# Kernel tuning notes

Hardware: AMD Instinct MI355X
Metric: run time of the kernel (lower is better)

Reference implementation:

```python
import jax, jax.numpy as jnp
import numpy as np

N = 50000       # nodes
E = 600000      # directed edges (before self loops)
IN_CH = 128
HID = 64
HEADS = 2
H2_CH = HID // HEADS  # 32
OUT_CH = 96
NEG_SLOPE = 0.2


def _w(key, shape):
    fan_in = shape[-1]
    return jax.random.normal(key, shape, dtype=jnp.float32) / np.sqrt(fan_in).astype(np.float32)


def setup_inputs() -> dict:
    key = jax.random.key(0)
    ks = jax.random.split(key, 20)
    x = jax.random.normal(ks[0], (N, IN_CH), dtype=jnp.float32)
    edge_index = jax.random.randint(ks[1], (2, E), 0, N, dtype=jnp.int32)
    batch = jnp.zeros((N,), dtype=jnp.int32)
    return {
        "x": x, "edge_index": edge_index, "batch": batch,
        # lin_in 128->128
        "Win": _w(ks[2], (IN_CH, IN_CH)), "b_in": jnp.zeros((IN_CH,), jnp.float32),
        # conv1: GATv2Conv(128 -> 64, heads=2, concat=True)
        "Wl1": _w(ks[3], (HEADS * HID, IN_CH)), "bl1": jnp.zeros((HEADS * HID,), jnp.float32),
        "Wr1": _w(ks[4], (HEADS * HID, IN_CH)), "br1": jnp.zeros((HEADS * HID,), jnp.float32),
        "att1": _w(ks[5], (HEADS, HID)), "bias1": jnp.zeros((HEADS * HID,), jnp.float32),
        # conv2: GATv2Conv(128 -> 32, heads=1, concat=True)
        "Wl2": _w(ks[6], (H2_CH, HEADS * HID)), "bl2": jnp.zeros((H2_CH,), jnp.float32),
        "Wr2": _w(ks[7], (H2_CH, HEADS * HID)), "br2": jnp.zeros((H2_CH,), jnp.float32),
        "att2": _w(ks[8], (1, H2_CH)), "bias2": jnp.zeros((H2_CH,), jnp.float32),
        # final linear 32 -> 96
        "Wout": _w(ks[9], (OUT_CH, H2_CH)), "b_out": jnp.zeros((OUT_CH,), jnp.float32),
    }


def _segment_softmax(logits, seg, num):
    # logits: [E, H] grouped by seg (destination node); every node has a self loop.
    m = jax.ops.segment_max(logits, seg, num_segments=num)
    ex = jnp.exp(logits - m[seg])
    s = jax.ops.segment_sum(ex, seg, num_segments=num)
    return ex / s[seg]


def _gatv2_conv(h, Wl, bl, Wr, br, att, bias, src, dst, heads, ch):
    n = h.shape[0]
    xl = (h @ Wl.T + bl).reshape(n, heads, ch)  # source-side (x_j)
    xr = (h @ Wr.T + br).reshape(n, heads, ch)  # target-side (x_i)
    e = jax.nn.leaky_relu(xl[src] + xr[dst], NEG_SLOPE)       # [E, H, C]
    logits = jnp.einsum('ehc,hc->eh', e, att)                  # [E, H]
    alpha = _segment_softmax(logits, dst, n)                   # softmax over in-edges per dst
    out = jax.ops.segment_sum(alpha[:, :, None] * xl[src], dst, num_segments=n)
    return out.reshape(n, heads * ch) + bias


def reference(x, edge_index, batch, Win, b_in, Wl1, bl1, Wr1, br1, att1, bias1,
              Wl2, bl2, Wr2, br2, att2, bias2, Wout, b_out):
    n = x.shape[0]
    loops = jnp.arange(n, dtype=edge_index.dtype)
    src = jnp.concatenate([edge_index[0], loops])  # add_self_loops=True (PyG default)
    dst = jnp.concatenate([edge_index[1], loops])
    h = x @ Win.T + b_in
    h = jax.nn.relu(_gatv2_conv(h, Wl1, bl1, Wr1, br1, att1, bias1, src, dst, HEADS, HID))
    h = jax.nn.relu(_gatv2_conv(h, Wl2, bl2, Wr2, br2, att2, bias2, src, dst, 1, H2_CH))
    num_graphs = 1
    sums = jax.ops.segment_sum(h, batch, num_segments=num_graphs)          # [G, 32]
    cnt = jax.ops.segment_sum(jnp.ones((n,), h.dtype), batch, num_segments=num_graphs)
    pooled = sums / cnt[:, None]
    return pooled @ Wout.T + b_out  # [G, 96]
```

## Files before the change

kernel.cpp:

```cpp
#include <hip/hip_runtime.h>
#include <hip/hip_bf16.h>
#include <math.h>


#define NEG_SLOPE 0.2f
#define LOG2E 1.4426950408889634f
#define NREP 16
#define ELLW 64
#define CH 2048
#define CAPB 8192

typedef __attribute__((ext_vector_type(8))) short bf16x8;
typedef __attribute__((ext_vector_type(4))) float f32x4;

__device__ __forceinline__ float leaky(float t) { return fmaxf(t, NEG_SLOPE * t); }
__device__ __forceinline__ float bf2f(unsigned short u) {
    return __uint_as_float((unsigned)u << 16);
}
__device__ __forceinline__ short f2bf(float f) {
    __hip_bfloat16 h = __float2bfloat16(f);
    return *reinterpret_cast<short*>(&h);
}
__device__ __forceinline__ short f2bf_fast(float f) {
    return (short)((__float_as_uint(f) + 0x8000u) >> 16);
}

__global__ __launch_bounds__(256) void prep_kernel(const float* __restrict__ Win,
                                                   const float* __restrict__ b_in,
                                                   const float* __restrict__ Wl1,
                                                   const float* __restrict__ bl1,
                                                   const float* __restrict__ Wr1,
                                                   const float* __restrict__ br1,
                                                   const float* __restrict__ Wl2,
                                                   const float* __restrict__ bl2,
                                                   const float* __restrict__ Wr2,
                                                   const float* __restrict__ br2,
                                                   unsigned short* __restrict__ Wcat1,
                                                   float* __restrict__ bcat1,
                                                   unsigned short* __restrict__ Wcat2,
                                                   float* __restrict__ bcat2,
                                                   int* __restrict__ bucketCnt,
                                                   float* __restrict__ pooledR, int N) {
    int b = blockIdx.x, t = threadIdx.x;
    if (b < 128) {
        int half = t >> 7;
        int k = t & 127;
        int o = b * 2 + half;
        const float* Wx = (o < 128) ? Wl1 : Wr1;
        const float* bx = (o < 128) ? bl1 : br1;
        int oo = o & 127;
        float acc = 0.f;
#pragma unroll 16
        for (int j = 0; j < 128; ++j)
            acc = fmaf(Wx[oo * 128 + j], Win[j * 128 + k], acc);
        Wcat1[o * 128 + k] = (unsigned short)f2bf(acc);

        __shared__ float red[256];
        red[t] = Wx[oo * 128 + k] * b_in[k];
        __syncthreads();
        for (int off = 64; off > 0; off >>= 1) {
            if (k < off) red[t] += red[t + off];
            __syncthreads();
        }
        if (k == 0) bcat1[o] = red[half * 128] + bx[oo];
    } else if (b < 160) {
        int i = (b - 128) * 256 + t;
        int m = i >> 7, kk = i & 127;
        float v = (m < 32) ? Wl2[m * 128 + kk] : Wr2[(m - 32) * 128 + kk];
        Wcat2[i] = (unsigned short)f2bf(v);
        if (b == 128 && t < 64) bcat2[t] = (t < 32) ? bl2[t] : br2[t - 32];
    } else if (b == 160) {
        if (t < 256) bucketCnt[t] = 0;
    } else {
        int i = (b - 161) * 256 + t;
        if (i < NREP * 32) pooledR[i] = 0.f;
    }
}

__global__ __launch_bounds__(256) void part_kernel(const int* __restrict__ ei,
                                                   int* __restrict__ bucketCnt,
                                                   unsigned int* __restrict__ region,
                                                   int E) {
    __shared__ int hist[256];
    __shared__ int base[256];
    __shared__ int off[256];
    int b = blockIdx.x, t = threadIdx.x;
    int e0 = b * CH;
    int e1 = e0 + CH; if (e1 > E) e1 = E;

    hist[t] = 0;
    __syncthreads();
    for (int e = e0 + t; e < e1; e += 256) {
        int d = ei[E + e];
        atomicAdd(&hist[d >> 8], 1);
    }
    __syncthreads();
    int h = hist[t];
    base[t] = (h > 0) ? atomicAdd(&bucketCnt[t], h) : 0;
    off[t] = 0;
    __syncthreads();
    for (int e = e0 + t; e < e1; e += 256) {
        int s = ei[e];
        int d = ei[E + e];
        int bk = d >> 8;
        int p = base[bk] + atomicAdd(&off[bk], 1);
        if (p < CAPB)
            region[(size_t)bk * CAPB + p] = (unsigned)s | ((unsigned)(d & 255) << 16);
    }
}

__global__ __launch_bounds__(256) void ellb_kernel(const unsigned int* __restrict__ region,
                                                   const int* __restrict__ bucketCnt,
                                                   unsigned short* __restrict__ ell,
                                                   int* __restrict__ deg, int N) {
    __shared__ unsigned short tile[256 * ELLW];
    __shared__ int cur[256];
    int nb = blockIdx.x, t = threadIdx.x;
    cur[t] = 0;
    __syncthreads();
    int cnt = bucketCnt[nb];
    if (cnt > CAPB) cnt = CAPB;
    for (int i = t; i < cnt; i += 256) {
        unsigned p = region[(size_t)nb * CAPB + i];
        int doff = p >> 16;
        int s = p & 0xFFFF;
        int r = atomicAdd(&cur[doff], 1);
        if (r < ELLW) tile[doff * ELLW + r] = (unsigned short)s;
    }
    __syncthreads();
    int node = nb * 256 + t;
    int dgl = cur[t];
    if (dgl > ELLW) dgl = ELLW;
    if (node < N) {
        deg[node] = dgl;
        int pe = dgl + 8; if (pe > ELLW) pe = ELLW;
        for (int r = dgl; r < pe; ++r) tile[t * ELLW + r] = (unsigned short)node;
    }
    __syncthreads();
    const uint4* tl = (const uint4*)tile;
    uint4* gl = (uint4*)(ell + (size_t)nb * 256 * ELLW);
#pragma unroll
    for (int k = 0; k < 8; ++k) {
        int idx = t + k * 256;
        int row = idx >> 3;
        if (nb * 256 + row < N) gl[idx] = tl[idx];
    }
}

__global__ __launch_bounds__(256) void gemm1_kernel(const float* __restrict__ x,
                                                    const unsigned short* __restrict__ W,
                                                    const float* __restrict__ bias,
                                                    unsigned short* __restrict__ XL,
                                                    unsigned short* __restrict__ XR, int N) {
    const int w = threadIdx.x >> 6;
    const int lane = threadIdx.x & 63;
    const int ln = lane & 15;
    const int quad = lane >> 4;
    const int nb = blockIdx.x * 32;
    const int c0 = w * 64;

    int rows[2];
#pragma unroll
    for (int rt = 0; rt < 2; ++rt) {
        int n = nb + rt * 16 + ln;
        rows[rt] = n < N ? n : N - 1;
    }

    float4 araw[2][4][2];
#pragma unroll
    for (int rt = 0; rt < 2; ++rt)
#pragma unroll
        for (int kc = 0; kc < 4; ++kc) {
            const float* p = x + (size_t)rows[rt] * 128 + kc * 32 + quad * 8;
            araw[rt][kc][0] = *(const float4*)p;
            araw[rt][kc][1] = *(const float4*)(p + 4);
        }
    bf16x8 a[2][4];
#pragma unroll
    for (int rt = 0; rt < 2; ++rt)
#pragma unroll
        for (int kc = 0; kc < 4; ++kc) {
            float4 u = araw[rt][kc][0], v = araw[rt][kc][1];
            a[rt][kc][0] = f2bf_fast(u.x); a[rt][kc][1] = f2bf_fast(u.y);
            a[rt][kc][2] = f2bf_fast(u.z); a[rt][kc][3] = f2bf_fast(u.w);
            a[rt][kc][4] = f2bf_fast(v.x); a[rt][kc][5] = f2bf_fast(v.y);
            a[rt][kc][6] = f2bf_fast(v.z); a[rt][kc][7] = f2bf_fast(v.w);
        }

    f32x4 acc[2][4];
#pragma unroll
    for (int rt = 0; rt < 2; ++rt)
#pragma unroll
        for (int ct = 0; ct < 4; ++ct) acc[rt][ct] = (f32x4){0.f, 0.f, 0.f, 0.f};

#pragma unroll
    for (int kc = 0; kc < 4; ++kc) {
        const int k0 = kc * 32 + quad * 8;
        bf16x8 wv[4];
#pragma unroll
        for (int ct = 0; ct < 4; ++ct)
            wv[ct] = *(const bf16x8*)(W + (size_t)(c0 + ct * 16 + ln) * 128 + k0);
#pragma unroll
        for (int rt = 0; rt < 2; ++rt)
#pragma unroll
            for (int ct = 0; ct < 4; ++ct)
                acc[rt][ct] = __builtin_amdgcn_mfma_f32_16x16x32_bf16(wv[ct], a[rt][kc], acc[rt][ct], 0, 0, 0);
    }

#pragma unroll
    for (int rt = 0; rt < 2; ++rt) {
        int n = nb + rt * 16 + ln;
        if (n >= N) continue;
#pragma unroll
        for (int ct = 0; ct < 4; ++ct) {
            int cb = c0 + ct * 16 + quad * 4;
            float4 bv = *(const float4*)&bias[cb];
            ushort4 o;
            o.x = (unsigned short)f2bf(acc[rt][ct][0] + bv.x);
            o.y = (unsigned short)f2bf(acc[rt][ct][1] + bv.y);
            o.z = (unsigned short)f2bf(acc[rt][ct][2] + bv.z);
            o.w = (unsigned short)f2bf(acc[rt][ct][3] + bv.w);
            if (cb < 128) *(ushort4*)&XL[(size_t)n * 128 + cb] = o;
            else          *(ushort4*)&XR[(size_t)n * 128 + cb - 128] = o;
        }
    }
}

__global__ __launch_bounds__(256) void node_conv1(const unsigned short* __restrict__ XL,
                                                  const unsigned short* __restrict__ XR,
                                                  const int* __restrict__ deg,
                                                  const unsigned short* __restrict__ ell,
                                                  const float* __restrict__ att,
                                                  const float* __restrict__ bias,
                                                  const unsigned short* __restrict__ Wcat2,
                                                  const float* __restrict__ bcat2,
                                                  unsigned short* __restrict__ XL2,
                                                  unsigned short* __restrict__ XR2, int N) {
    __shared__ unsigned short hsh[8 * 128];
    int g = threadIdx.x >> 5;
    int d = blockIdx.x * 8 + g;
    int l = threadIdx.x & 31;
    int c0 = 4 * l;

    if (d < N) {
        const unsigned short* row = ell + (size_t)d * ELLW;
        int re = deg[d];

        float4 attv = *(const float4*)&att[c0];
        attv.x *= LOG2E; attv.y *= LOG2E; attv.z *= LOG2E; attv.w *= LOG2E;
        ushort4 xru = *(const ushort4*)&XR[(size_t)d * 128 + c0];
        float xr0 = bf2f(xru.x), xr1 = bf2f(xru.y), xr2 = bf2f(xru.z), xr3 = bf2f(xru.w);

        float ssum = 0.f, a0 = 0.f, a1 = 0.f, a2 = 0.f, a3 = 0.f;

#define LOADX1(j) (*(const ushort4*)&XL[(size_t)row[j] * 128 + c0])
#define PROC1(xu)                                                          \
    {                                                                      \
        float x0 = bf2f(xu.x), x1 = bf2f(xu.y), x2 = bf2f(xu.z), x3 = bf2f(xu.w); \
        float p = leaky(x0 + xr0) * attv.x;                                \
        p = fmaf(leaky(x1 + xr1), attv.y, p);                              \
        p = fmaf(leaky(x2 + xr2), attv.z, p);                              \
        p = fmaf(leaky(x3 + xr3), attv.w, p);                              \
        p += __shfl_xor(p, 8, 16);                                         \
        p += __shfl_xor(p, 4, 16);                                         \
        p += __shfl_xor(p, 2, 16);                                         \
        p += __shfl_xor(p, 1, 16);                                         \
        float wgt = exp2f(p);                                              \
        ssum += wgt;                                                       \
        a0 = fmaf(wgt, x0, a0); a1 = fmaf(wgt, x1, a1);                    \
        a2 = fmaf(wgt, x2, a2); a3 = fmaf(wgt, x3, a3);                    \
    }

        {
            ushort4 xls = *(const ushort4*)&XL[(size_t)d * 128 + c0];
            PROC1(xls);
        }
        if (re > 0) {
            ushort4 b0 = LOADX1(0), b1 = LOADX1(1), b2 = LOADX1(2), b3 = LOADX1(3);
            for (int j = 0; j < re; j += 4) {
                int j4 = j + 4 < ELLW - 3 ? j + 4 : ELLW - 4;
                ushort4 n0 = LOADX1(j4), n1 = LOADX1(j4 + 1), n2 = LOADX1(j4 + 2), n3 = LOADX1(j4 + 3);
                PROC1(b0);
                if (j + 1 < re) PROC1(b1);
                if (j + 2 < re) PROC1(b2);
                if (j + 3 < re) PROC1(b3);
                b0 = n0; b1 = n1; b2 = n2; b3 = n3;
            }
        }
#undef PROC1
#undef LOADX1

        float inv = 1.0f / ssum;
        float4 bv = *(const float4*)&bias[c0];
        float r0 = fmaf(a0, inv, bv.x), r1 = fmaf(a1, inv, bv.y);
        float r2 = fmaf(a2, inv, bv.z), r3 = fmaf(a3, inv, bv.w);
        ushort4 o;
        o.x = (unsigned short)f2bf(r0 > 0.f ? r0 : 0.f);
        o.y = (unsigned short)f2bf(r1 > 0.f ? r1 : 0.f);
        o.z = (unsigned short)f2bf(r2 > 0.f ? r2 : 0.f);
        o.w = (unsigned short)f2bf(r3 > 0.f ? r3 : 0.f);
        *(ushort4*)&hsh[g * 128 + c0] = o;
    } else {
        *(ushort4*)&hsh[g * 128 + c0] = make_ushort4(0, 0, 0, 0);
    }
    __syncthreads();

    {
        int w = threadIdx.x >> 6;
        int lane = threadIdx.x & 63;
        int ln = lane & 15;
        int quad = lane >> 4;
        f32x4 acc = (f32x4){0.f, 0.f, 0.f, 0.f};
#pragma unroll
        for (int kc = 0; kc < 4; ++kc) {
            int k0 = kc * 32 + quad * 8;
            bf16x8 a;
            if (ln < 8) a = *(const bf16x8*)&hsh[ln * 128 + k0];
            else        a = (bf16x8){0, 0, 0, 0, 0, 0, 0, 0};
            bf16x8 wv = *(const bf16x8*)(Wcat2 + (size_t)(w * 16 + ln) * 128 + k0);
            acc = __builtin_amdgcn_mfma_f32_16x16x32_bf16(wv, a, acc, 0, 0, 0);
        }
        int n = blockIdx.x * 8 + ln;
        if (ln < 8 && n < N) {
            int cb = w * 16 + quad * 4;
            float4 bv = *(const float4*)&bcat2[cb];
            ushort4 o;
            o.x = (unsigned short)f2bf(acc[0] + bv.x);
            o.y = (unsigned short)f2bf(acc[1] + bv.y);
            o.z = (unsigned short)f2bf(acc[2] + bv.z);
            o.w = (unsigned short)f2bf(acc[3] + bv.w);
            if (cb < 32) *(ushort4*)&XL2[(size_t)n * 32 + cb] = o;
            else         *(ushort4*)&XR2[(size_t)n * 32 + cb - 32] = o;
        }
    }
}

__global__ __launch_bounds__(256) void node_conv2(const unsigned short* __restrict__ XL,
                                                  const unsigned short* __restrict__ XR,
                                                  const int* __restrict__ deg,
                                                  const unsigned short* __restrict__ ell,
                                                  const float* __restrict__ att,
                                                  const float* __restrict__ bias,
                                                  float* __restrict__ pooledR, int N) {
    __shared__ float psh[32];
    if (threadIdx.x < 32) psh[threadIdx.x] = 0.0f;
    __syncthreads();

    int slot = threadIdx.x >> 3;
    int l = threadIdx.x & 7;
    int c0 = 4 * l;
    float4 attv = *(const float4*)&att[c0];
    attv.x *= LOG2E; attv.y *= LOG2E; attv.z *= LOG2E; attv.w *= LOG2E;
    float4 bv = *(const float4*)&bias[c0];
    float p0 = 0.f, p1 = 0.f, p2 = 0.f, p3 = 0.f;

#define LOADX2(j) (*(const ushort4*)&XL[(size_t)row[j] * 32 + c0])
#define PROC2(xu)                                                          \
    {                                                                      \
        float x0 = bf2f(xu.x), x1 = bf2f(xu.y), x2 = bf2f(xu.z), x3 = bf2f(xu.w); \
        float p = leaky(x0 + xr0) * attv.x;                                \
        p = fmaf(leaky(x1 + xr1), attv.y, p);                              \
        p = fmaf(leaky(x2 + xr2), attv.z, p);                              \
        p = fmaf(leaky(x3 + xr3), attv.w, p);                              \
        p += __shfl_xor(p, 4, 8);                                          \
        p += __shfl_xor(p, 2, 8);                                          \
        p += __shfl_xor(p, 1, 8);                                          \
        float wgt = exp2f(p);                                              \
        ssum += wgt;                                                       \
        a0 = fmaf(wgt, x0, a0); a1 = fmaf(wgt, x1, a1);                    \
        a2 = fmaf(wgt, x2, a2); a3 = fmaf(wgt, x3, a3);                    \
    }

    for (int d = blockIdx.x * 32 + slot; d < N; d += gridDim.x * 32) {
        const unsigned short* row = ell + (size_t)d * ELLW;
        int re = deg[d];
        ushort4 xru = *(const ushort4*)&XR[(size_t)d * 32 + c0];
        float xr0 = bf2f(xru.x), xr1 = bf2f(xru.y), xr2 = bf2f(xru.z), xr3 = bf2f(xru.w);
        float ssum = 0.f, a0 = 0.f, a1 = 0.f, a2 = 0.f, a3 = 0.f;

        {
            ushort4 xls = *(const ushort4*)&XL[(size_t)d * 32 + c0];
            PROC2(xls);
        }
        if (re > 0) {
            ushort4 b0 = LOADX2(0), b1 = LOADX2(1), b2 = LOADX2(2), b3 = LOADX2(3);
            for (int j = 0; j < re; j += 4) {
                int j4 = j + 4 < ELLW - 3 ? j + 4 : ELLW - 4;
                ushort4 n0 = LOADX2(j4), n1 = LOADX2(j4 + 1), n2 = LOADX2(j4 + 2), n3 = LOADX2(j4 + 3);
                PROC2(b0);
                if (j + 1 < re) PROC2(b1);
                if (j + 2 < re) PROC2(b2);
                if (j + 3 < re) PROC2(b3);
                b0 = n0; b1 = n1; b2 = n2; b3 = n3;
            }
        }

        float inv = 1.0f / ssum;
        float r0 = fmaf(a0, inv, bv.x), r1 = fmaf(a1, inv, bv.y);
        float r2 = fmaf(a2, inv, bv.z), r3 = fmaf(a3, inv, bv.w);
        p0 += r0 > 0.f ? r0 : 0.f;
        p1 += r1 > 0.f ? r1 : 0.f;
        p2 += r2 > 0.f ? r2 : 0.f;
        p3 += r3 > 0.f ? r3 : 0.f;
    }
#undef PROC2
#undef LOADX2
    atomicAdd(&psh[c0 + 0], p0);
    atomicAdd(&psh[c0 + 1], p1);
    atomicAdd(&psh[c0 + 2], p2);
    atomicAdd(&psh[c0 + 3], p3);
    __syncthreads();
    float* rep = pooledR + (blockIdx.x & (NREP - 1)) * 32;
    if (threadIdx.x < 32) atomicAdd(&rep[threadIdx.x], psh[threadIdx.x]);
}

__global__ void out_kernel(const float* __restrict__ pooledR, const float* __restrict__ Wout,
                           const float* __restrict__ b_out, float* __restrict__ out, int N) {
    __shared__ float psum[32];
    if (threadIdx.x < 32) {
        float tot = 0.f;
#pragma unroll
        for (int r = 0; r < NREP; ++r) tot += pooledR[r * 32 + threadIdx.x];
        psum[threadIdx.x] = tot;
    }
    __syncthreads();
    int m = threadIdx.x;
    if (m < 96) {
        float invN = 1.0f / (float)N;
        float s = b_out[m];
#pragma unroll
        for (int c = 0; c < 32; ++c) s += (psum[c] * invN) * Wout[m * 32 + c];
        out[m] = s;
    }
}

extern "C" void kernel_launch(void* const* d_in, const int* in_sizes, int n_in,
                              void* d_out, int out_size, void* d_ws, size_t ws_size,
                              hipStream_t stream) {
    const float* x     = (const float*)d_in[0];
    const int*   ei    = (const int*)d_in[1];
    const float* Win   = (const float*)d_in[3];
    const float* b_in  = (const float*)d_in[4];
    const float* Wl1   = (const float*)d_in[5];
    const float* bl1   = (const float*)d_in[6];
    const float* Wr1   = (const float*)d_in[7];
    const float* br1   = (const float*)d_in[8];
    const float* att1  = (const float*)d_in[9];
    const float* bias1 = (const float*)d_in[10];
    const float* Wl2   = (const float*)d_in[11];
    const float* bl2   = (const float*)d_in[12];
    const float* Wr2   = (const float*)d_in[13];
    const float* br2   = (const float*)d_in[14];
    const float* att2  = (const float*)d_in[15];
    const float* bias2 = (const float*)d_in[16];
    const float* Wout  = (const float*)d_in[17];
    const float* b_out = (const float*)d_in[18];
    float* out = (float*)d_out;

    int N = in_sizes[0] / 128;
    int E = in_sizes[1] / 2;
    int NB = (N + 255) >> 8;

    char* wsb = (char*)d_ws;
    size_t off = 0;
    auto alloc = [&](size_t bytes) { void* p = wsb + off; off += (bytes + 255) & ~(size_t)255; return p; };

    unsigned short* XL1   = (unsigned short*)alloc((size_t)N * 128 * 2);
    unsigned short* XR1   = (unsigned short*)alloc((size_t)N * 128 * 2);
    unsigned short* XL2   = (unsigned short*)alloc((size_t)N * 32 * 2);
    unsigned short* XR2   = (unsigned short*)alloc((size_t)N * 32 * 2);
    unsigned short* Wcat1 = (unsigned short*)alloc(256 * 128 * 2);
    unsigned short* Wcat2 = (unsigned short*)alloc(64 * 128 * 2);
    float* bcat1   = (float*)alloc(256 * 4);
    float* bcat2   = (float*)alloc(64 * 4);
    float* pooledR = (float*)alloc(NREP * 32 * 4);
    int* bucketCnt = (int*)alloc(256 * 4);
    int* deg       = (int*)alloc((size_t)N * 4);
    unsigned int* region = (unsigned int*)alloc((size_t)NB * CAPB * 4);
    unsigned short* ell  = (unsigned short*)alloc((size_t)N * ELLW * 2);

    prep_kernel<<<163, 256, 0, stream>>>(Win, b_in, Wl1, bl1, Wr1, br1,
                                         Wl2, bl2, Wr2, br2,
                                         Wcat1, bcat1, Wcat2, bcat2, bucketCnt, pooledR, N);
    part_kernel<<<(E + CH - 1) / CH, 256, 0, stream>>>(ei, bucketCnt, region, E);
    ellb_kernel<<<NB, 256, 0, stream>>>(region, bucketCnt, ell, deg, N);
    gemm1_kernel<<<(N + 31) / 32, 256, 0, stream>>>(x, Wcat1, bcat1, XL1, XR1, N);
    node_conv1<<<(N + 7) / 8, 256, 0, stream>>>(XL1, XR1, deg, ell, att1, bias1,
                                                Wcat2, bcat2, XL2, XR2, N);
    node_conv2<<<1024, 256, 0, stream>>>(XL2, XR2, deg, ell, att2, bias2, pooledR, N);
    out_kernel<<<1, 128, 0, stream>>>(pooledR, Wout, b_out, out, N);
}
```

Before: 224.6 us.

## Use DPP reductions, vectorized ELL index loads, and branchless padded-edge correction

Replaces the shfl_xor-based head reductions in both GATv2 aggregation kernels with DPP row/quad permute adds, which avoids LDS-routed shuffles. ELL neighbor indices are now read four at a time as ushort4. The per-edge validity branches are removed: padded slots, assumed to hold the self index, are processed unconditionally, and their contribution is subtracted afterwards using the self-loop weight. This relies on the ELL padding convention and on the DPP control codes matching the intended lane groupings, and the subtraction may slightly change floating-point rounding.

```diff
diff --git a/kernel.cpp b/kernel.cpp
--- a/kernel.cpp
+++ b/kernel.cpp
@@ -23,6 +23,12 @@
 }
 __device__ __forceinline__ short f2bf_fast(float f) {
     return (short)((__float_as_uint(f) + 0x8000u) >> 16);
+}
+
+template <int CTRL>
+__device__ __forceinline__ float dppadd(float v) {
+    int t = __builtin_amdgcn_update_dpp(0, __float_as_int(v), CTRL, 0xF, 0xF, true);
+    return v + __int_as_float(t);
 }
 
 __global__ __launch_bounds__(256) void prep_kernel(const float* __restrict__ Win,
@@ -251,9 +257,10 @@
         ushort4 xru = *(const ushort4*)&XR[(size_t)d * 128 + c0];
         float xr0 = bf2f(xru.x), xr1 = bf2f(xru.y), xr2 = bf2f(xru.z), xr3 = bf2f(xru.w);
 
-        float ssum = 0.f, a0 = 0.f, a1 = 0.f, a2 = 0.f, a3 = 0.f;
-
-#define LOADX1(j) (*(const ushort4*)&XL[(size_t)row[j] * 128 + c0])
+        float ssum, a0, a1, a2, a3;
+        float w_self, xs0, xs1, xs2, xs3;
+
+#define LOADX1(s) (*(const ushort4*)&XL[(size_t)(s) * 128 + c0])
 #define PROC1(xu)                                                          \
     {                                                                      \
         float x0 = bf2f(xu.x), x1 = bf2f(xu.y), x2 = bf2f(xu.z), x3 = bf2f(xu.w); \
@@ -261,10 +268,10 @@
         p = fmaf(leaky(x1 + xr1), attv.y, p);                              \
         p = fmaf(leaky(x2 + xr2), attv.z, p);                              \
         p = fmaf(leaky(x3 + xr3), attv.w, p);                              \
-        p += __shfl_xor(p, 8, 16);                                         \
-        p += __shfl_xor(p, 4, 16);                                         \
-        p += __shfl_xor(p, 2, 16);                                         \
-        p += __shfl_xor(p, 1, 16);                                         \
+        p = dppadd<0xB1>(p);                                               \
+        p = dppadd<0x4E>(p);                                               \
+        p = dppadd<0x124>(p);                                              \
+        p = dppadd<0x128>(p);                                              \
         float wgt = exp2f(p);                                              \
         ssum += wgt;                                                       \
         a0 = fmaf(wgt, x0, a0); a1 = fmaf(wgt, x1, a1);                    \
@@ -272,20 +279,39 @@
     }
 
         {
-            ushort4 xls = *(const ushort4*)&XL[(size_t)d * 128 + c0];
-            PROC1(xls);
+            ushort4 xu = *(const ushort4*)&XL[(size_t)d * 128 + c0];
+            xs0 = bf2f(xu.x); xs1 = bf2f(xu.y); xs2 = bf2f(xu.z); xs3 = bf2f(xu.w);
+            float p = leaky(xs0 + xr0) * attv.x;
+            p = fmaf(leaky(xs1 + xr1), attv.y, p);
+            p = fmaf(leaky(xs2 + xr2), attv.z, p);
+            p = fmaf(leaky(xs3 + xr3), attv.w, p);
+            p = dppadd<0xB1>(p);
+            p = dppadd<0x4E>(p);
+            p = dppadd<0x124>(p);
+            p = dppadd<0x128>(p);
+            w_self = exp2f(p);
+            ssum = w_self;
+            a0 = w_self * xs0; a1 = w_self * xs1;
+            a2 = w_self * xs2; a3 = w_self * xs3;
         }
         if (re > 0) {
-            ushort4 b0 = LOADX1(0), b1 = LOADX1(1), b2 = LOADX1(2), b3 = LOADX1(3);
-            for (int j = 0; j < re; j += 4) {
+            int rp = (re + 3) & ~3;
+            ushort4 i0 = *(const ushort4*)&row[0];
+            ushort4 b0 = LOADX1(i0.x), b1 = LOADX1(i0.y), b2 = LOADX1(i0.z), b3 = LOADX1(i0.w);
+            for (int j = 0; j < rp; j += 4) {
                 int j4 = j + 4 < ELLW - 3 ? j + 4 : ELLW - 4;
-                ushort4 n0 = LOADX1(j4), n1 = LOADX1(j4 + 1), n2 = LOADX1(j4 + 2), n3 = LOADX1(j4 + 3);
+                ushort4 i1 = *(const ushort4*)&row[j4];
+                ushort4 n0 = LOADX1(i1.x), n1 = LOADX1(i1.y), n2 = LOADX1(i1.z), n3 = LOADX1(i1.w);
                 PROC1(b0);
-                if (j + 1 < re) PROC1(b1);
-                if (j + 2 < re) PROC1(b2);
-                if (j + 3 < re) PROC1(b3);
+                PROC1(b1);
+                PROC1(b2);
+                PROC1(b3);
                 b0 = n0; b1 = n1; b2 = n2; b3 = n3;
             }
+            float kw = (float)(rp - re) * w_self;
+            ssum -= kw;
+            a0 = fmaf(-kw, xs0, a0); a1 = fmaf(-kw, xs1, a1);
+            a2 = fmaf(-kw, xs2, a2); a3 = fmaf(-kw, xs3, a3);
         }
 #undef PROC1
 #undef LOADX1
@@ -354,7 +380,7 @@
     float4 bv = *(const float4*)&bias[c0];
     float p0 = 0.f, p1 = 0.f, p2 = 0.f, p3 = 0.f;
 
-#define LOADX2(j) (*(const ushort4*)&XL[(size_t)row[j] * 32 + c0])
+#define LOADX2(s) (*(const ushort4*)&XL[(size_t)(s) * 32 + c0])
 #define PROC2(xu)                                                          \
     {                                                                      \
         float x0 = bf2f(xu.x), x1 = bf2f(xu.y), x2 = bf2f(xu.z), x3 = bf2f(xu.w); \
@@ -362,9 +388,9 @@
         p = fmaf(leaky(x1 + xr1), attv.y, p);                              \
         p = fmaf(leaky(x2 + xr2), attv.z, p);                              \
         p = fmaf(leaky(x3 + xr3), attv.w, p);                              \
-        p += __shfl_xor(p, 4, 8);                                          \
-        p += __shfl_xor(p, 2, 8);                                          \
-        p += __shfl_xor(p, 1, 8);                                          \
+        p = dppadd<0xB1>(p);                                               \
+        p = dppadd<0x4E>(p);                                               \
+        p = dppadd<0x141>(p);                                              \
         float wgt = exp2f(p);                                              \
         ssum += wgt;                                                       \
         a0 = fmaf(wgt, x0, a0); a1 = fmaf(wgt, x1, a1);                    \
@@ -376,23 +402,42 @@
         int re = deg[d];
         ushort4 xru = *(const ushort4*)&XR[(size_t)d * 32 + c0];
         float xr0 = bf2f(xru.x), xr1 = bf2f(xru.y), xr2 = bf2f(xru.z), xr3 = bf2f(xru.w);
-        float ssum = 0.f, a0 = 0.f, a1 = 0.f, a2 = 0.f, a3 = 0.f;
+        float ssum, a0, a1, a2, a3;
+        float w_self, xs0, xs1, xs2, xs3;
 
         {
-            ushort4 xls = *(const ushort4*)&XL[(size_t)d * 32 + c0];
-            PROC2(xls);
+            ushort4 xu = *(const ushort4*)&XL[(size_t)d * 32 + c0];
+            xs0 = bf2f(xu.x); xs1 = bf2f(xu.y); xs2 = bf2f(xu.z); xs3 = bf2f(xu.w);
+            float p = leaky(xs0 + xr0) * attv.x;
+            p = fmaf(leaky(xs1 + xr1), attv.y, p);
+            p = fmaf(leaky(xs2 + xr2), attv.z, p);
+            p = fmaf(leaky(xs3 + xr3), attv.w, p);
+            p = dppadd<0xB1>(p);
+            p = dppadd<0x4E>(p);
+            p = dppadd<0x141>(p);
+            w_self = exp2f(p);
+            ssum = w_self;
+            a0 = w_self * xs0; a1 = w_self * xs1;
+            a2 = w_self * xs2; a3 = w_self * xs3;
         }
         if (re > 0) {
-            ushort4 b0 = LOADX2(0), b1 = LOADX2(1), b2 = LOADX2(2), b3 = LOADX2(3);
-            for (int j = 0; j < re; j += 4) {
+            int rp = (re + 3) & ~3;
+            ushort4 i0 = *(const ushort4*)&row[0];
+            ushort4 b0 = LOADX2(i0.x), b1 = LOADX2(i0.y), b2 = LOADX2(i0.z), b3 = LOADX2(i0.w);
+            for (int j = 0; j < rp; j += 4) {
                 int j4 = j + 4 < ELLW - 3 ? j + 4 : ELLW - 4;
-                ushort4 n0 = LOADX2(j4), n1 = LOADX2(j4 + 1), n2 = LOADX2(j4 + 2), n3 = LOADX2(j4 + 3);
+                ushort4 i1 = *(const ushort4*)&row[j4];
+                ushort4 n0 = LOADX2(i1.x), n1 = LOADX2(i1.y), n2 = LOADX2(i1.z), n3 = LOADX2(i1.w);
                 PROC2(b0);
-                if (j + 1 < re) PROC2(b1);
-                if (j + 2 < re) PROC2(b2);
-                if (j + 3 < re) PROC2(b3);
+                PROC2(b1);
+                PROC2(b2);
+                PROC2(b3);
                 b0 = n0; b1 = n1; b2 = n2; b3 = n3;
             }
+            float kw = (float)(rp - re) * w_self;
+            ssum -= kw;
+            a0 = fmaf(-kw, xs0, a0); a1 = fmaf(-kw, xs1, a1);
+            a2 = fmaf(-kw, xs2, a2); a3 = fmaf(-kw, xs3, a3);
         }
 
         float inv = 1.0f / ssum;
```

Measured after the change: 213.1 us. 5.1% less time.
